# Optimization experiments

Measured on AMD Instinct MI355X. Metric: run time of the kernel, lower is better.

## Reference

```python
import jax, jax.numpy as jnp
import numpy as np
import math

N = 262144
D_K = 64
D_V = 64


def setup_inputs() -> dict:
    key = jax.random.key(0)
    kq, kk, kv = jax.random.split(key, 3)
    Q = jax.random.normal(kq, (N, D_K), dtype=jnp.float32)
    K = jax.random.normal(kk, (N, D_K), dtype=jnp.float32)
    V = jax.random.normal(kv, (N, D_V), dtype=jnp.float32)
    return {"Q": Q, "K": K, "V": V}


def reference(Q, K, V):
    d_k = Q.shape[-1]
    scale = 1.0 / math.sqrt(d_k)
    # rho_q: softmax over the sequence axis (dim=-2)
    q = jax.nn.softmax(Q * scale, axis=-2)  # [N, d_k]
    # rho_k: softmax over the feature axis (dim=-1)
    k = jax.nn.softmax(K * scale, axis=-1)  # [N, d_k]
    # linear attention: [d_k, d_v] context first, then project with q
    context = k.T @ V                        # [d_k, d_v]
    return q @ context                       # [N, d_v]
```

## Files before the change

kernel.cpp:

```cpp
#include <hip/hip_runtime.h>
#include <hip/hip_bf16.h>

#define NROWS 262144
#define B1 512
#define RPB 512
#define CL 0.18033688011112042f

typedef __attribute__((ext_vector_type(8))) short s8v;
typedef __attribute__((ext_vector_type(4))) float f4v;

__device__ __forceinline__ ushort f2bf(float x) {
    unsigned u = __float_as_uint(x);
    u += 0x7FFF + ((u >> 16) & 1);
    return (ushort)(u >> 16);
}

__device__ __forceinline__ float dpp_red16(float x) {
    int t;
    t = __builtin_amdgcn_update_dpp(0, __float_as_int(x), 0xB1,  0xF, 0xF, true);
    x += __int_as_float(t);
    t = __builtin_amdgcn_update_dpp(0, __float_as_int(x), 0x4E,  0xF, 0xF, true);
    x += __int_as_float(t);
    t = __builtin_amdgcn_update_dpp(0, __float_as_int(x), 0x141, 0xF, 0xF, true);
    x += __int_as_float(t);
    t = __builtin_amdgcn_update_dpp(0, __float_as_int(x), 0x140, 0xF, 0xF, true);
    x += __int_as_float(t);
    return x;
}

__global__ __launch_bounds__(512, 4) void k1_stats(const float* __restrict__ Q,
                                                   const float* __restrict__ K,
                                                   const float* __restrict__ V,
                                                   float* __restrict__ ctx_part,
                                                   float* __restrict__ qs_part)
{
    const int tid  = threadIdx.x;
    const int lane = tid & 63;
    const int wid  = tid >> 6;
    const size_t base = (size_t)blockIdx.x * RPB;

    __shared__ ushort kkT[2][64 * 64];
    __shared__ ushort vT [2][64 * 64];
    __shared__ float  qsl[8 * 64];

    const int cb  = wid >> 1;
    const int vb0 = (wid & 1) * 2;
    f4v acc0 = {0.f, 0.f, 0.f, 0.f};
    f4v acc1 = {0.f, 0.f, 0.f, 0.f};
    float qs = 0.f;

    const unsigned wr_off = (unsigned)lane * 128u + (unsigned)((wid ^ (lane & 7)) << 4);
    const int li = lane & 15, g = lane >> 4;

    const float* kp = K + (base + wid * 8) * 64 + lane;
    const float* vp = V + (base + wid * 8) * 64 + lane;
    const float* qp = Q + (base + wid * 8) * 64 + lane;

    float kr[8], vr[8], qr[8];
#pragma unroll
    for (int i = 0; i < 8; ++i) kr[i] = kp[i * 64];
#pragma unroll
    for (int i = 0; i < 8; ++i) vr[i] = vp[i * 64];
#pragma unroll
    for (int i = 0; i < 8; ++i) qr[i] = qp[i * 64];

    for (int ch = 0; ch < 8; ++ch) {
        float nkr[8], nvr[8], nqr[8];
        if (ch < 7) {
            const float* kp2 = kp + (size_t)(ch + 1) * 4096;
            const float* vp2 = vp + (size_t)(ch + 1) * 4096;
            const float* qp2 = qp + (size_t)(ch + 1) * 4096;
#pragma unroll
            for (int i = 0; i < 8; ++i) nkr[i] = kp2[i * 64];
#pragma unroll
            for (int i = 0; i < 8; ++i) nvr[i] = vp2[i * 64];
#pragma unroll
            for (int i = 0; i < 8; ++i) nqr[i] = qp2[i * 64];
        }
        float e[8], s[8];
#pragma unroll
        for (int i = 0; i < 8; ++i) e[i] = exp2f(kr[i] * CL);
#pragma unroll
        for (int i = 0; i < 8; ++i) s[i] = dpp_red16(e[i]);
#pragma unroll
        for (int i = 0; i < 8; ++i) s[i] += __shfl_xor(s[i], 16);
#pragma unroll
        for (int i = 0; i < 8; ++i) s[i] += __shfl_xor(s[i], 32);

        s8v kvp, vvp;
#pragma unroll
        for (int i = 0; i < 8; ++i) {
            kvp[i] = (short)f2bf(e[i] * __builtin_amdgcn_rcpf(s[i]));
            vvp[i] = (short)f2bf(vr[i]);
            qs += exp2f(qr[i] * CL);
        }
        const int p = ch & 1;
        *(s8v*)((char*)kkT[p] + wr_off) = kvp;
        *(s8v*)((char*)vT[p]  + wr_off) = vvp;
        __syncthreads();
#pragma unroll
        for (int ks = 0; ks < 2; ++ks) {
            const int G  = ks * 4 + g;
            const int ca = cb  * 16 + li;
            const int c0 = vb0 * 16 + li;
            s8v a  = *(const s8v*)((const char*)kkT[p] + ca * 128 + ((G ^ (ca & 7)) << 4));
            s8v b0 = *(const s8v*)((const char*)vT[p]  + c0 * 128 + ((G ^ (c0 & 7)) << 4));
            s8v b1 = *(const s8v*)((const char*)vT[p]  + (c0 + 16) * 128 + ((G ^ (c0 & 7)) << 4));
            acc0 = __builtin_amdgcn_mfma_f32_16x16x32_bf16(a, b0, acc0, 0, 0, 0);
            acc1 = __builtin_amdgcn_mfma_f32_16x16x32_bf16(a, b1, acc1, 0, 0, 0);
        }
        if (ch < 7) {
#pragma unroll
            for (int i = 0; i < 8; ++i) { kr[i] = nkr[i]; vr[i] = nvr[i]; qr[i] = nqr[i]; }
        }
    }
#pragma unroll
    for (int r = 0; r < 4; ++r) {
        const int row = cb * 16 + g * 4 + r;
        ctx_part[(size_t)blockIdx.x * 4096 + row * 64 + vb0 * 16 + li]       = acc0[r];
        ctx_part[(size_t)blockIdx.x * 4096 + row * 64 + (vb0 + 1) * 16 + li] = acc1[r];
    }
    qsl[wid * 64 + lane] = qs;
    __syncthreads();
    if (tid < 64) {
        float s = 0.f;
#pragma unroll
        for (int w = 0; w < 8; ++w) s += qsl[w * 64 + tid];
        qs_part[blockIdx.x * 64 + tid] = s;
    }
}

__global__ __launch_bounds__(256) void k2(const float* __restrict__ ctx_part,
                                          const float* __restrict__ qs_part,
                                          ushort* __restrict__ ctxfT) {
    const int c = blockIdx.x;
    const int tid = threadIdx.x;
    const int v = tid & 63;
    const int g = tid >> 6;
    __shared__ float red[4][64];
    __shared__ float qred[4][64];
    float s = 0.f;
    for (int b = g; b < B1; b += 4) s += ctx_part[(size_t)b * 4096 + c * 64 + v];
    float q = 0.f;
    for (int b = tid; b < B1; b += 256) q += qs_part[b * 64 + c];
    red[g][v] = s;
    qred[g][v] = q;
    __syncthreads();
    if (tid < 64) {
        float t  = (red[0][v] + red[1][v]) + (red[2][v] + red[3][v]);
        float qv = (qred[0][v] + qred[1][v]) + (qred[2][v] + qred[3][v]);
        qv = dpp_red16(qv);
        qv += __shfl_xor(qv, 16);
        qv += __shfl_xor(qv, 32);
        ctxfT[v * 64 + c] = f2bf(t * __builtin_amdgcn_rcpf(qv));
    }
}

__global__ __launch_bounds__(256) void k3_out(const float* __restrict__ Q,
                                              const ushort* __restrict__ ctxfT,
                                              float* __restrict__ out) {
    const int tid  = threadIdx.x;
    const int lane = tid & 63;
    const int wid  = tid >> 6;
    const int li = lane & 15, g = lane >> 4;

    s8v bfr[4][2];
#pragma unroll
    for (int vb = 0; vb < 4; ++vb)
#pragma unroll
        for (int ks = 0; ks < 2; ++ks)
            bfr[vb][ks] = *(const s8v*)((const char*)ctxfT +
                            2 * ((vb * 16 + li) * 64 + 32 * ks + 8 * g));

#pragma unroll
    for (int t = 0; t < 4; ++t) {
        const int rb  = blockIdx.x * 256 + t * 64 + wid * 16;
        const int row = rb + li;
        const f4v* qp = (const f4v*)(Q + (size_t)row * 64);
        f4v q0 = qp[2 * g], q1 = qp[2 * g + 1];
        f4v q2 = qp[8 + 2 * g], q3 = qp[8 + 2 * g + 1];
        s8v a0, a1;
#pragma unroll
        for (int e = 0; e < 4; ++e) {
            a0[e]     = (short)f2bf(exp2f(q0[e] * CL));
            a0[e + 4] = (short)f2bf(exp2f(q1[e] * CL));
            a1[e]     = (short)f2bf(exp2f(q2[e] * CL));
            a1[e + 4] = (short)f2bf(exp2f(q3[e] * CL));
        }
#pragma unroll
        for (int vb = 0; vb < 4; ++vb) {
            f4v acc = {0.f, 0.f, 0.f, 0.f};
            acc = __builtin_amdgcn_mfma_f32_16x16x32_bf16(a0, bfr[vb][0], acc, 0, 0, 0);
            acc = __builtin_amdgcn_mfma_f32_16x16x32_bf16(a1, bfr[vb][1], acc, 0, 0, 0);
#pragma unroll
            for (int r = 0; r < 4; ++r)
                out[(size_t)(rb + g * 4 + r) * 64 + vb * 16 + li] = acc[r];
        }
    }
}

extern "C" void kernel_launch(void* const* d_in, const int* in_sizes, int n_in,
                              void* d_out, int out_size, void* d_ws, size_t ws_size,
                              hipStream_t stream) {
    const float* Q = (const float*)d_in[0];
    const float* K = (const float*)d_in[1];
    const float* V = (const float*)d_in[2];
    float* out = (float*)d_out;

    float* w = (float*)d_ws;
    size_t off = 0;
    float*  qs_part = w + off;              off += (size_t)B1 * 64;
    ushort* ctxfT   = (ushort*)(w + off);   off += 2048;
    float* ctx_part;
    const size_t need = (off + (size_t)B1 * 4096) * sizeof(float);
    if (ws_size >= need) {
        ctx_part = w + off;
    } else {
        ctx_part = out;
    }

    k1_stats<<<B1, 512, 0, stream>>>(Q, K, V, ctx_part, qs_part);
    k2<<<64, 256, 0, stream>>>(ctx_part, qs_part, ctxfT);
    k3_out<<<NROWS / 256, 256, 0, stream>>>(Q, ctxfT, out);
}
```

Baseline: 92.54 us.

## Split Q column-sum into own kernel and DMA K/V via LDS triple buffer

After: 102.4 us. 1.11x slower.

```diff
diff --git a/kernel.cpp b/kernel.cpp
--- a/kernel.cpp
+++ b/kernel.cpp
@@ -2,6 +2,7 @@
 #include <hip/hip_bf16.h>
 
 #define NROWS 262144
+#define B0 2048
 #define B1 512
 #define RPB 512
 #define CL 0.18033688011112042f
@@ -28,76 +29,113 @@
     return x;
 }
 
-__global__ __launch_bounds__(512, 4) void k1_stats(const float* __restrict__ Q,
-                                                   const float* __restrict__ K,
-                                                   const float* __restrict__ V,
-                                                   float* __restrict__ ctx_part,
-                                                   float* __restrict__ qs_part)
+__device__ __forceinline__ void dma16(const float* g, float* l) {
+    __builtin_amdgcn_global_load_lds(
+        (const __attribute__((address_space(1))) unsigned int*)g,
+        (__attribute__((address_space(3))) unsigned int*)l, 16, 0, 0);
+}
+
+__global__ __launch_bounds__(256) void k0_qsum(const float* __restrict__ Q,
+                                               float* __restrict__ q_part) {
+    const int tid  = threadIdx.x;
+    const int lane = tid & 63;
+    const int wid  = tid >> 6;
+    const int t    = blockIdx.x * 256 + tid;
+    const f4v* q4  = (const f4v*)Q;
+    float a0 = 0.f, a1 = 0.f, a2 = 0.f, a3 = 0.f;
+#pragma unroll 4
+    for (int f = t; f < NROWS * 16; f += B0 * 256) {
+        f4v v = q4[f];
+        a0 += exp2f(v[0] * CL); a1 += exp2f(v[1] * CL);
+        a2 += exp2f(v[2] * CL); a3 += exp2f(v[3] * CL);
+    }
+    a0 += __shfl_xor(a0, 16); a0 += __shfl_xor(a0, 32);
+    a1 += __shfl_xor(a1, 16); a1 += __shfl_xor(a1, 32);
+    a2 += __shfl_xor(a2, 16); a2 += __shfl_xor(a2, 32);
+    a3 += __shfl_xor(a3, 16); a3 += __shfl_xor(a3, 32);
+    __shared__ float part[4][64];
+    if (lane < 16) {
+        part[wid][4 * lane + 0] = a0; part[wid][4 * lane + 1] = a1;
+        part[wid][4 * lane + 2] = a2; part[wid][4 * lane + 3] = a3;
+    }
+    __syncthreads();
+    if (tid < 64)
+        q_part[blockIdx.x * 64 + tid] =
+            (part[0][tid] + part[1][tid]) + (part[2][tid] + part[3][tid]);
+}
+
+__global__ __launch_bounds__(512) void k1_stats(const float* __restrict__ K,
+                                                const float* __restrict__ V,
+                                                float* __restrict__ ctx_part)
 {
     const int tid  = threadIdx.x;
     const int lane = tid & 63;
     const int wid  = tid >> 6;
     const size_t base = (size_t)blockIdx.x * RPB;
 
-    __shared__ ushort kkT[2][64 * 64];
-    __shared__ ushort vT [2][64 * 64];
-    __shared__ float  qsl[8 * 64];
+    __shared__ float  rawK[3][4096];
+    __shared__ float  rawV[3][4096];
+    __shared__ ushort kkT[2][4096];
+    __shared__ ushort vT [2][4096];
 
     const int cb  = wid >> 1;
     const int vb0 = (wid & 1) * 2;
     f4v acc0 = {0.f, 0.f, 0.f, 0.f};
     f4v acc1 = {0.f, 0.f, 0.f, 0.f};
-    float qs = 0.f;
 
     const unsigned wr_off = (unsigned)lane * 128u + (unsigned)((wid ^ (lane & 7)) << 4);
     const int li = lane & 15, g = lane >> 4;
-
-    const float* kp = K + (base + wid * 8) * 64 + lane;
-    const float* vp = V + (base + wid * 8) * 64 + lane;
-    const float* qp = Q + (base + wid * 8) * 64 + lane;
-
-    float kr[8], vr[8], qr[8];
-#pragma unroll
-    for (int i = 0; i < 8; ++i) kr[i] = kp[i * 64];
-#pragma unroll
-    for (int i = 0; i < 8; ++i) vr[i] = vp[i * 64];
-#pragma unroll
-    for (int i = 0; i < 8; ++i) qr[i] = qp[i * 64];
-
+    const int lsrc = (lane >> 4) * 64 + (lane & 15) * 4;
+    const int ldst = wid * 512;
+
+#define ISSUE(ch) do { \
+        const int _s = (ch) % 3; \
+        const float* kb = K + (base + (size_t)(ch) * 64 + wid * 8) * 64; \
+        const float* vb = V + (base + (size_t)(ch) * 64 + wid * 8) * 64; \
+        dma16(kb + lsrc,       &rawK[_s][ldst]); \
+        dma16(kb + 256 + lsrc, &rawK[_s][ldst + 256]); \
+        dma16(vb + lsrc,       &rawV[_s][ldst]); \
+        dma16(vb + 256 + lsrc, &rawV[_s][ldst + 256]); \
+    } while (0)
+
+    ISSUE(0); ISSUE(1); ISSUE(2);
+
+#pragma unroll
     for (int ch = 0; ch < 8; ++ch) {
-        float nkr[8], nvr[8], nqr[8];
-        if (ch < 7) {
-            const float* kp2 = kp + (size_t)(ch + 1) * 4096;
-            const float* vp2 = vp + (size_t)(ch + 1) * 4096;
-            const float* qp2 = qp + (size_t)(ch + 1) * 4096;
-#pragma unroll
-            for (int i = 0; i < 8; ++i) nkr[i] = kp2[i * 64];
-#pragma unroll
-            for (int i = 0; i < 8; ++i) nvr[i] = vp2[i * 64];
-#pragma unroll
-            for (int i = 0; i < 8; ++i) nqr[i] = qp2[i * 64];
-        }
-        float e[8], s[8];
+        if (ch <= 5)      asm volatile("s_waitcnt vmcnt(8)" ::: "memory");
+        else if (ch == 6) asm volatile("s_waitcnt vmcnt(4)" ::: "memory");
+        else              asm volatile("s_waitcnt vmcnt(0)" ::: "memory");
+        const int s = ch % 3, p = ch & 1;
+
+        float kr[8], vr[8];
+#pragma unroll
+        for (int i = 0; i < 8; ++i) kr[i] = rawK[s][ldst + i * 64 + lane];
+#pragma unroll
+        for (int i = 0; i < 8; ++i) vr[i] = rawV[s][ldst + i * 64 + lane];
+
+        float e[8], sm[8];
 #pragma unroll
         for (int i = 0; i < 8; ++i) e[i] = exp2f(kr[i] * CL);
 #pragma unroll
-        for (int i = 0; i < 8; ++i) s[i] = dpp_red16(e[i]);
-#pragma unroll
-        for (int i = 0; i < 8; ++i) s[i] += __shfl_xor(s[i], 16);
-#pragma unroll
-        for (int i = 0; i < 8; ++i) s[i] += __shfl_xor(s[i], 32);
+        for (int i = 0; i < 8; ++i) sm[i] = dpp_red16(e[i]);
+#pragma unroll
+        for (int i = 0; i < 8; ++i) sm[i] += __shfl_xor(sm[i], 16);
+#pragma unroll
+        for (int i = 0; i < 8; ++i) sm[i] += __shfl_xor(sm[i], 32);
 
         s8v kvp, vvp;
 #pragma unroll
         for (int i = 0; i < 8; ++i) {
-            kvp[i] = (short)f2bf(e[i] * __builtin_amdgcn_rcpf(s[i]));
+            kvp[i] = (short)f2bf(e[i] * __builtin_amdgcn_rcpf(sm[i]));
             vvp[i] = (short)f2bf(vr[i]);
-            qs += exp2f(qr[i] * CL);
-        }
-        const int p = ch & 1;
+        }
         *(s8v*)((char*)kkT[p] + wr_off) = kvp;
         *(s8v*)((char*)vT[p]  + wr_off) = vvp;
-        __syncthreads();
+        asm volatile("s_waitcnt lgkmcnt(0)" ::: "memory");
+        if (ch < 5) ISSUE(ch + 3);
+        __builtin_amdgcn_s_barrier();
+        asm volatile("" ::: "memory");
+
 #pragma unroll
         for (int ks = 0; ks < 2; ++ks) {
             const int G  = ks * 4 + g;
@@ -109,29 +147,18 @@
             acc0 = __builtin_amdgcn_mfma_f32_16x16x32_bf16(a, b0, acc0, 0, 0, 0);
             acc1 = __builtin_amdgcn_mfma_f32_16x16x32_bf16(a, b1, acc1, 0, 0, 0);
         }
-        if (ch < 7) {
-#pragma unroll
-            for (int i = 0; i < 8; ++i) { kr[i] = nkr[i]; vr[i] = nvr[i]; qr[i] = nqr[i]; }
-        }
-    }
+    }
+#undef ISSUE
 #pragma unroll
     for (int r = 0; r < 4; ++r) {
         const int row = cb * 16 + g * 4 + r;
         ctx_part[(size_t)blockIdx.x * 4096 + row * 64 + vb0 * 16 + li]       = acc0[r];
         ctx_part[(size_t)blockIdx.x * 4096 + row * 64 + (vb0 + 1) * 16 + li] = acc1[r];
     }
-    qsl[wid * 64 + lane] = qs;
-    __syncthreads();
-    if (tid < 64) {
-        float s = 0.f;
-#pragma unroll
-        for (int w = 0; w < 8; ++w) s += qsl[w * 64 + tid];
-        qs_part[blockIdx.x * 64 + tid] = s;
-    }
 }
 
 __global__ __launch_bounds__(256) void k2(const float* __restrict__ ctx_part,
-                                          const float* __restrict__ qs_part,
+                                          const float* __restrict__ q_part,
                                           ushort* __restrict__ ctxfT) {
     const int c = blockIdx.x;
     const int tid = threadIdx.x;
@@ -142,7 +169,7 @@
     float s = 0.f;
     for (int b = g; b < B1; b += 4) s += ctx_part[(size_t)b * 4096 + c * 64 + v];
     float q = 0.f;
-    for (int b = tid; b < B1; b += 256) q += qs_part[b * 64 + c];
+    for (int b = tid; b < B0; b += 256) q += q_part[b * 64 + c];
     red[g][v] = s;
     qred[g][v] = q;
     __syncthreads();
@@ -209,8 +236,8 @@
 
     float* w = (float*)d_ws;
     size_t off = 0;
-    float*  qs_part = w + off;              off += (size_t)B1 * 64;
-    ushort* ctxfT   = (ushort*)(w + off);   off += 2048;
+    float*  q_part = w + off;               off += (size_t)B0 * 64;
+    ushort* ctxfT  = (ushort*)(w + off);    off += 2048;
     float* ctx_part;
     const size_t need = (off + (size_t)B1 * 4096) * sizeof(float);
     if (ws_size >= need) {
@@ -219,7 +246,8 @@
         ctx_part = out;
     }
 
-    k1_stats<<<B1, 512, 0, stream>>>(Q, K, V, ctx_part, qs_part);
-    k2<<<64, 256, 0, stream>>>(ctx_part, qs_part, ctxfT);
+    k1_stats<<<B1, 512, 0, stream>>>(K, V, ctx_part);
+    k0_qsum<<<B0, 256, 0, stream>>>(Q, q_part);
+    k2<<<64, 256, 0, stream>>>(ctx_part, q_part, ctxfT);
     k3_out<<<NROWS / 256, 256, 0, stream>>>(Q, ctxfT, out);
 }
```
